# Kernel tuning notes

Measured on AMD Instinct MI355X. Metric: run time of the kernel, lower is better.

Reference implementation:

```python
import jax, jax.numpy as jnp
import numpy as np

N_HEAD = 16
EPS = 1e-6

def hypersphere_norm(x, g):
    # unit-normalize on hidden dim, rescale to sqrt(d), learnable gain
    d = x.shape[-1]
    n = jnp.linalg.norm(x, axis=-1, keepdims=True)
    return (x / (n + EPS)) * jnp.sqrt(jnp.asarray(d, x.dtype)) * g


def setup_inputs() -> dict:
    key = jax.random.key(0)
    ks = jax.random.split(key, 8)
    B, S, D, F = 2, 2048, 2048, 8192
    s = lambda fan: 1.0 / np.sqrt(fan)
    return {
        "hidden_states": jax.random.normal(ks[0], (B, S, D), jnp.float32),
        "Wq": jax.random.normal(ks[1], (D, D), jnp.float32) * s(D),
        "Wk": jax.random.normal(ks[2], (D, D), jnp.float32) * s(D),
        "Wv": jax.random.normal(ks[3], (D, D), jnp.float32) * s(D),
        "Wo": jax.random.normal(ks[4], (D, D), jnp.float32) * s(D),
        "W_in": jax.random.normal(ks[5], (F, D), jnp.float32) * s(D),
        "W_out": jax.random.normal(ks[6], (D, F), jnp.float32) * s(F),
        "qk_norm_factor": jnp.asarray(1.0 / np.sqrt(D // N_HEAD), jnp.float32),
        "g_attn": jnp.ones((D,), jnp.float32),
        "g_mlp": jnp.ones((D,), jnp.float32),
    }


def reference(hidden_states, Wq, Wk, Wv, Wo, W_in, W_out, qk_norm_factor, g_attn, g_mlp):
    B, S, D = hidden_states.shape
    H = N_HEAD
    hd = D // H

    # ---- pre-attn hypersphere norm ----
    residual = hidden_states
    x = hypersphere_norm(hidden_states, g_attn)

    def shape_heads(t):  # [B,S,D] -> [B,H,S,hd]
        return t.reshape(B, S, H, hd).transpose(0, 2, 1, 3)

    q = shape_heads(x @ Wq.T)
    k = shape_heads(x @ Wk.T)
    v = shape_heads(x @ Wv.T)

    # QK-norm: unit-normalize per head vector
    q = q / (jnp.linalg.norm(q, axis=-1, keepdims=True) + EPS)
    k = k / (jnp.linalg.norm(k, axis=-1, keepdims=True) + EPS)

    scores = jnp.einsum("bhqd,bhkd->bhqk", q, k) * qk_norm_factor
    causal = jnp.tril(jnp.ones((S, S), bool))
    scores = jnp.where(causal[None, None], scores, jnp.asarray(-jnp.inf, scores.dtype))
    probs = jax.nn.softmax(scores, axis=-1)
    attn = jnp.einsum("bhqk,bhkd->bhqd", probs, v)  # [B,H,S,hd]
    attn = attn.transpose(0, 2, 1, 3).reshape(B, S, D)
    attn = attn @ Wo.T  # dropout=0

    h = residual + attn

    # ---- MLP branch ----
    residual = h
    y = hypersphere_norm(h, g_mlp)
    y = jax.nn.gelu(y @ W_in.T, approximate=False)
    y = y @ W_out.T
    return residual + y
```

## Files before the change

### kernel.cpp

```cpp
#include <hip/hip_runtime.h>
#include <math.h>


typedef unsigned short ushort_t;
typedef __attribute__((ext_vector_type(8))) short short8;
typedef __attribute__((ext_vector_type(4))) short short4v;
typedef __attribute__((ext_vector_type(4))) float f32x4;

#define S_LEN 2048
#define D_DIM 2048
#define F_DIM 8192
#define NHEAD 16
#define HDIM 128
#define BATCH 2
#define MROWS (BATCH * S_LEN)

__device__ __forceinline__ float bf2f(ushort_t u) {
  union { unsigned int i; float f; } c; c.i = ((unsigned int)u) << 16; return c.f;
}
__device__ __forceinline__ ushort_t f2bf(float f) {
  union { unsigned int i; float f; } c; c.f = f;
  unsigned int u = c.i;
  unsigned int r = (u + 0x7FFFu + ((u >> 16) & 1u)) >> 16;
  return (ushort_t)r;
}
__device__ __forceinline__ void load_lds16(const ushort_t* g, ushort_t* l) {
  __builtin_amdgcn_global_load_lds((const __attribute__((address_space(1))) void*)g,
                                   (__attribute__((address_space(3))) void*)l,
                                   16, 0, 0);
}

__global__ __launch_bounds__(256) void f2b_all_kernel(const float* __restrict__ wq,
                                                      const float* __restrict__ wk,
                                                      const float* __restrict__ wv,
                                                      const float* __restrict__ wo,
                                                      const float* __restrict__ wi,
                                                      const float* __restrict__ wu,
                                                      ushort_t* __restrict__ out) {
  const size_t DD = (size_t)D_DIM * D_DIM;
  const size_t FD = (size_t)F_DIM * D_DIM;
  const size_t e = ((size_t)blockIdx.x * 256 + threadIdx.x) * 4;
  const float* src;
  size_t off;
  if (e < 4 * DD) {
    const int wsel = (int)(e >> 22);
    src = (wsel == 0) ? wq : (wsel == 1) ? wk : (wsel == 2) ? wv : wo;
    off = e & (DD - 1);
  } else if (e < 4 * DD + FD) {
    src = wi; off = e - 4 * DD;
  } else {
    src = wu; off = e - 4 * DD - FD;
  }
  float4 v = *(const float4*)(src + off);
  short4v o;
  o[0] = (short)f2bf(v.x); o[1] = (short)f2bf(v.y);
  o[2] = (short)f2bf(v.z); o[3] = (short)f2bf(v.w);
  *(short4v*)(out + e) = o;
}

__global__ __launch_bounds__(256) void hsnorm_kernel(const float* __restrict__ x,
                                                     const float* __restrict__ g,
                                                     ushort_t* __restrict__ out) {
  const int row = blockIdx.x;
  const int t = threadIdx.x;
  const size_t base = (size_t)row * D_DIM + t * 8;
  float4 x0 = *(const float4*)(x + base);
  float4 x1 = *(const float4*)(x + base + 4);
  float f[8] = {x0.x, x0.y, x0.z, x0.w, x1.x, x1.y, x1.z, x1.w};
  float ss = 0.f;
#pragma unroll
  for (int j = 0; j < 8; ++j) ss += f[j] * f[j];
#pragma unroll
  for (int o = 32; o >= 1; o >>= 1) ss += __shfl_xor(ss, o);
  __shared__ float red[4];
  if ((t & 63) == 0) red[t >> 6] = ss;
  __syncthreads();
  const float tot = red[0] + red[1] + red[2] + red[3];
  const float factor = 45.254833995939045f / (sqrtf(tot) + 1e-6f);
  float4 g0 = *(const float4*)(g + t * 8);
  float4 g1 = *(const float4*)(g + t * 8 + 4);
  float gg[8] = {g0.x, g0.y, g0.z, g0.w, g1.x, g1.y, g1.z, g1.w};
  short8 ov;
#pragma unroll
  for (int j = 0; j < 8; ++j) ov[j] = (short)f2bf(f[j] * factor * gg[j]);
  *(short8*)(out + base) = ov;
}

__global__ __launch_bounds__(256) void qknorm_kernel(ushort_t* __restrict__ buf, float scale) {
  const int wv = threadIdx.x >> 6;
  const int lane = threadIdx.x & 63;
  const size_t vi = (size_t)blockIdx.x * 4 + wv;
  ushort_t* p = buf + vi * 128 + lane * 2;
  const float a = bf2f(p[0]), b = bf2f(p[1]);
  float ss = a * a + b * b;
#pragma unroll
  for (int o = 32; o >= 1; o >>= 1) ss += __shfl_xor(ss, o);
  const float f = scale / (sqrtf(ss) + 1e-6f);
  p[0] = f2bf(a * f);
  p[1] = f2bf(b * f);
}

template <int EPI>
__global__ __launch_bounds__(256) void gemm_bt(const ushort_t* __restrict__ A,
                                               const ushort_t* __restrict__ W,
                                               const float* __restrict__ RES,
                                               void* __restrict__ Cv,
                                               int M, int N, int K) {
  __shared__ __align__(16) ushort_t a_lds[128 * 64];
  __shared__ __align__(16) ushort_t b_lds[128 * 64];
  const int tid = threadIdx.x;
  const int w = tid >> 6;
  const int lane = tid & 63;
  const int quad = lane >> 4;
  const int l15 = lane & 15;
  const int wr = w >> 1, wc = w & 1;
  const long bm = (long)blockIdx.x * 128;
  const long bn = (long)blockIdx.y * 128;

  const int srow = tid >> 2;
  const int scol = (tid & 3) * 8;
  const ushort_t* gA = A + (size_t)(bm + srow) * K + scol;
  const ushort_t* gB = W + (size_t)(bn + srow) * K + scol;
  ushort_t* lA = a_lds + w * 512;
  ushort_t* lB = b_lds + w * 512;
  const size_t half = (size_t)64 * K;

  f32x4 acc[4][4] = {};

  for (int k0 = 0; k0 < K; k0 += 64) {
    load_lds16(gA,             lA);
    load_lds16(gA + half,      lA + 2048);
    load_lds16(gB,             lB);
    load_lds16(gB + half,      lB + 2048);
    load_lds16(gA + 32,        lA + 4096);
    load_lds16(gA + 32 + half, lA + 6144);
    load_lds16(gB + 32,        lB + 4096);
    load_lds16(gB + 32 + half, lB + 6144);
    gA += 64; gB += 64;
    __syncthreads();
#pragma unroll
    for (int kk = 0; kk < 2; ++kk) {
      short8 af[4], bfr[4];
#pragma unroll
      for (int i = 0; i < 4; ++i) {
        af[i]  = *(const short8*)&a_lds[kk * 4096 + (wr * 64 + i * 16 + l15) * 32 + quad * 8];
        bfr[i] = *(const short8*)&b_lds[kk * 4096 + (wc * 64 + i * 16 + l15) * 32 + quad * 8];
      }
#pragma unroll
      for (int i = 0; i < 4; ++i)
#pragma unroll
        for (int j = 0; j < 4; ++j)
          acc[i][j] = __builtin_amdgcn_mfma_f32_16x16x32_bf16(af[i], bfr[j], acc[i][j], 0, 0, 0);
    }
    __syncthreads();
  }

  const size_t SZq = (size_t)MROWS * D_DIM;
#pragma unroll
  for (int i = 0; i < 4; ++i) {
    const long row0 = bm + wr * 64 + i * 16 + quad * 4;
#pragma unroll
    for (int j = 0; j < 4; ++j) {
      const long col = bn + wc * 64 + j * 16 + l15;
      if (EPI == 4) {
        if (col < 4096) {
          ushort_t* dst = (ushort_t*)Cv + (col < 2048 ? 0 : SZq);
          const long c = col & (D_DIM - 1);
#pragma unroll
          for (int r = 0; r < 4; ++r)
            dst[(size_t)(row0 + r) * D_DIM + c] = f2bf(acc[i][j][r]);
        } else {
          const long b = row0 >> 11;
          const long s0 = row0 & (S_LEN - 1);
          const long h = (col >> 7) & 15;
          const long d = col & (HDIM - 1);
          short4v ov;
#pragma unroll
          for (int r = 0; r < 4; ++r) ov[r] = (short)f2bf(acc[i][j][r]);
          *(short4v*)((ushort_t*)Cv + 2 * SZq + ((b * NHEAD + h) * HDIM + d) * S_LEN + s0) = ov;
        }
      } else {
#pragma unroll
        for (int r = 0; r < 4; ++r) {
          float v = acc[i][j][r];
          const size_t idx = (size_t)(row0 + r) * N + col;
          if (EPI == 1) {
            ((float*)Cv)[idx] = v + RES[idx];
          } else if (EPI == 2) {
            v = 0.5f * v * (1.0f + erff(v * 0.70710678118654752f));
            ((ushort_t*)Cv)[idx] = f2bf(v);
          }
        }
      }
    }
  }
}

__global__ __launch_bounds__(256) void attn_kernel(const ushort_t* __restrict__ q,
                                                   const ushort_t* __restrict__ k,
                                                   const ushort_t* __restrict__ vt,
                                                   ushort_t* __restrict__ out) {
  __shared__ __align__(16) ushort_t K_lds[64 * 128];
  __shared__ __align__(16) ushort_t Vt_lds[128 * 64];
  __shared__ __align__(16) ushort_t P_lds[4 * 16 * 64];
  const int tid = threadIdx.x;
  const int w = tid >> 6;
  const int lane = tid & 63;
  const int quad = lane >> 4;
  const int l15 = lane & 15;

  const int qt = (S_LEN / 64 - 1) - (blockIdx.x & (S_LEN / 64 - 1));
  const int bh = blockIdx.x >> 5;
  const int b = bh >> 4;
  const int h = bh & 15;
  const int q0 = qt * 64;
  const int wrow0 = q0 + w * 16;
  const size_t base = ((size_t)b * S_LEN) * D_DIM + h * HDIM;
  const size_t vtbase = ((size_t)(b * NHEAD + h)) * HDIM * S_LEN;

  short8 qa[4];
#pragma unroll
  for (int st = 0; st < 4; ++st)
    qa[st] = *(const short8*)(q + base + (size_t)(wrow0 + l15) * D_DIM + st * 32 + quad * 8);

  const int kc0 = w * 64 + lane;
  ushort_t* Pw = P_lds + w * 1024;

  f32x4 o[8] = {};
  float m[4], l[4];
#pragma unroll
  for (int r = 0; r < 4; ++r) { m[r] = -__builtin_inff(); l[r] = 0.f; }

  const int ktmax = (q0 + 63) >> 6;
  for (int kt = 0; kt <= ktmax; ++kt) {
#pragma unroll
    for (int r2 = 0; r2 < 4; ++r2) {
      const int c = r2 * 256 + kc0;
      {
        const int db = c >> 8, key = (c >> 2) & 63, dl = (c & 3) * 8;
        load_lds16(k + base + (size_t)(kt * 64 + key) * D_DIM + db * 32 + dl,
                   K_lds + (size_t)(r2 * 4 + w) * 512);
      }
      {
        const int kc = c >> 9, d = (c >> 2) & 127, kl = (c & 3) * 8;
        load_lds16(vt + vtbase + (size_t)d * S_LEN + kt * 64 + kc * 32 + kl,
                   Vt_lds + (size_t)(r2 * 4 + w) * 512);
      }
    }
    __syncthreads();

    if (kt * 64 <= wrow0 + 15) {
      f32x4 s[4];
#pragma unroll
      for (int h2 = 0; h2 < 4; ++h2) {
        f32x4 sa = {};
#pragma unroll
        for (int st = 0; st < 4; ++st) {
          short8 kb = *(const short8*)&K_lds[st * 2048 + (h2 * 16 + l15) * 32 + quad * 8];
          sa = __builtin_amdgcn_mfma_f32_16x16x32_bf16(qa[st], kb, sa, 0, 0, 0);
        }
        s[h2] = sa;
      }

      const int kbase = kt * 64 + l15;
      float alpha[4];
#pragma unroll
      for (int r = 0; r < 4; ++r) {
        const int qrow = wrow0 + quad * 4 + r;
        float sv[4];
#pragma unroll
        for (int h2 = 0; h2 < 4; ++h2)
          sv[h2] = (kbase + h2 * 16 <= qrow) ? s[h2][r] : -__builtin_inff();
        float tmax = fmaxf(fmaxf(sv[0], sv[1]), fmaxf(sv[2], sv[3]));
#pragma unroll
        for (int off = 8; off >= 1; off >>= 1) tmax = fmaxf(tmax, __shfl_xor(tmax, off));
        const float mn = fmaxf(m[r], tmax);
        const float al = __expf(m[r] - mn);
        float p[4], ps = 0.f;
#pragma unroll
        for (int h2 = 0; h2 < 4; ++h2) { p[h2] = __expf(sv[h2] - mn); ps += p[h2]; }
#pragma unroll
        for (int off = 8; off >= 1; off >>= 1) ps += __shfl_xor(ps, off);
        l[r] = l[r] * al + ps;
        m[r] = mn;
        alpha[r] = al;
#pragma unroll
        for (int h2 = 0; h2 < 4; ++h2)
          Pw[(h2 >> 1) * 512 + (quad * 4 + r) * 32 + (h2 & 1) * 16 + l15] = f2bf(p[h2]);
      }

#pragma unroll
      for (int c = 0; c < 8; ++c)
#pragma unroll
        for (int r = 0; r < 4; ++r) o[c][r] *= alpha[r];

      short8 af0 = *(const short8*)&Pw[l15 * 32 + quad * 8];
      short8 af1 = *(const short8*)&Pw[512 + l15 * 32 + quad * 8];
#pragma unroll
      for (int c = 0; c < 8; ++c) {
        short8 vb0 = *(const short8*)&Vt_lds[(c * 16 + l15) * 32 + quad * 8];
        o[c] = __builtin_amdgcn_mfma_f32_16x16x32_bf16(af0, vb0, o[c], 0, 0, 0);
        short8 vb1 = *(const short8*)&Vt_lds[4096 + (c * 16 + l15) * 32 + quad * 8];
        o[c] = __builtin_amdgcn_mfma_f32_16x16x32_bf16(af1, vb1, o[c], 0, 0, 0);
      }
    }
    __syncthreads();
  }

#pragma unroll
  for (int c = 0; c < 8; ++c)
#pragma unroll
    for (int r = 0; r < 4; ++r) {
      const float val = o[c][r] / l[r];
      out[base + (size_t)(wrow0 + quad * 4 + r) * D_DIM + c * 16 + l15] = f2bf(val);
    }
}

extern "C" void kernel_launch(void* const* d_in, const int* in_sizes, int n_in,
                              void* d_out, int out_size, void* d_ws, size_t ws_size,
                              hipStream_t stream) {
  const float* hid  = (const float*)d_in[0];
  const float* Wq   = (const float*)d_in[1];
  const float* Wk   = (const float*)d_in[2];
  const float* Wv   = (const float*)d_in[3];
  const float* Wo   = (const float*)d_in[4];
  const float* Win  = (const float*)d_in[5];
  const float* Wout = (const float*)d_in[6];
  const float* ga   = (const float*)d_in[8];
  const float* gm   = (const float*)d_in[9];
  float* out = (float*)d_out;

  const size_t DD = (size_t)D_DIM * D_DIM;
  const size_t FD = (size_t)F_DIM * D_DIM;
  const size_t SZ = (size_t)MROWS * D_DIM;

  ushort_t* wqb  = (ushort_t*)d_ws;
  ushort_t* wob  = wqb + 3 * DD;
  ushort_t* winb = wob + DD;
  ushort_t* woutb= winb + FD;
  float*    hb   = (float*)(woutb + FD);
  ushort_t* qb   = (ushort_t*)(hb + SZ);
  ushort_t* kb   = qb + SZ;
  ushort_t* vtb  = kb + SZ;
  ushort_t* xb   = vtb + SZ;
  ushort_t* mid  = kb;

  f2b_all_kernel<<<(unsigned)((4 * DD + 2 * FD) / 1024), 256, 0, stream>>>(
      Wq, Wk, Wv, Wo, Win, Wout, wqb);

  hsnorm_kernel<<<MROWS, 256, 0, stream>>>(hid, ga, xb);
  gemm_bt<4><<<dim3(MROWS / 128, 6144 / 128), 256, 0, stream>>>(
      xb, wqb, nullptr, qb, MROWS, 6144, D_DIM);
  qknorm_kernel<<<(MROWS * NHEAD) / 4, 256, 0, stream>>>(qb, 0.08838834764831845f);
  qknorm_kernel<<<(MROWS * NHEAD) / 4, 256, 0, stream>>>(kb, 1.0f);
  attn_kernel<<<BATCH * NHEAD * (S_LEN / 64), 256, 0, stream>>>(qb, kb, vtb, xb);
  gemm_bt<1><<<dim3(MROWS / 128, D_DIM / 128), 256, 0, stream>>>(
      xb, wob, hid, hb, MROWS, D_DIM, D_DIM);
  hsnorm_kernel<<<MROWS, 256, 0, stream>>>(hb, gm, qb);
  gemm_bt<2><<<dim3(MROWS / 128, F_DIM / 128), 256, 0, stream>>>(
      qb, winb, nullptr, mid, MROWS, F_DIM, D_DIM);
  gemm_bt<1><<<dim3(MROWS / 128, D_DIM / 128), 256, 0, stream>>>(
      mid, woutb, hb, out, MROWS, D_DIM, F_DIM);
}
```

Before: 994.7 us.

## Replace GEMM with 256x256-tile, double-buffered, swizzled-LDS 8-wave kernel

Replaces the 128x128 single-buffered GEMM with a 256x256 tile kernel using 512 threads, 128KB of dynamic LDS, and ping-pong buffers for the A and B stages. It adds XOR swizzling to avoid LDS bank conflicts, interleaves global-to-LDS loads with MFMA phases, and uses s_setprio around the compute sections. The goal is more data reuse per loaded byte and hiding memory latency behind compute. The trade-offs are higher register and LDS pressure and fewer blocks for the smaller GEMMs, e.g. 16x8 blocks for the D-by-D projections.

```diff
diff --git a/kernel.cpp b/kernel.cpp
--- a/kernel.cpp
+++ b/kernel.cpp
@@ -28,6 +28,9 @@
   __builtin_amdgcn_global_load_lds((const __attribute__((address_space(1))) void*)g,
                                    (__attribute__((address_space(3))) void*)l,
                                    16, 0, 0);
+}
+__device__ __forceinline__ f32x4 mf(short8 a, short8 b, f32x4 c) {
+  return __builtin_amdgcn_mfma_f32_16x16x32_bf16(a, b, c, 0, 0, 0);
 }
 
 __global__ __launch_bounds__(256) void f2b_all_kernel(const float* __restrict__ wq,
@@ -101,64 +104,148 @@
 }
 
 template <int EPI>
-__global__ __launch_bounds__(256) void gemm_bt(const ushort_t* __restrict__ A,
-                                               const ushort_t* __restrict__ W,
-                                               const float* __restrict__ RES,
-                                               void* __restrict__ Cv,
-                                               int M, int N, int K) {
-  __shared__ __align__(16) ushort_t a_lds[128 * 64];
-  __shared__ __align__(16) ushort_t b_lds[128 * 64];
+__global__ __launch_bounds__(512, 2) void gemm256(const ushort_t* __restrict__ A,
+                                                  const ushort_t* __restrict__ W,
+                                                  const float* __restrict__ RES,
+                                                  void* __restrict__ Cv,
+                                                  int M, int N, int K) {
+  extern __shared__ char smem[];
   const int tid = threadIdx.x;
   const int w = tid >> 6;
   const int lane = tid & 63;
   const int quad = lane >> 4;
   const int l15 = lane & 15;
-  const int wr = w >> 1, wc = w & 1;
-  const long bm = (long)blockIdx.x * 128;
-  const long bn = (long)blockIdx.y * 128;
-
-  const int srow = tid >> 2;
-  const int scol = (tid & 3) * 8;
-  const ushort_t* gA = A + (size_t)(bm + srow) * K + scol;
-  const ushort_t* gB = W + (size_t)(bn + srow) * K + scol;
-  ushort_t* lA = a_lds + w * 512;
-  ushort_t* lB = b_lds + w * 512;
-  const size_t half = (size_t)64 * K;
-
-  f32x4 acc[4][4] = {};
-
-  for (int k0 = 0; k0 < K; k0 += 64) {
-    load_lds16(gA,             lA);
-    load_lds16(gA + half,      lA + 2048);
-    load_lds16(gB,             lB);
-    load_lds16(gB + half,      lB + 2048);
-    load_lds16(gA + 32,        lA + 4096);
-    load_lds16(gA + 32 + half, lA + 6144);
-    load_lds16(gB + 32,        lB + 4096);
-    load_lds16(gB + 32 + half, lB + 6144);
-    gA += 64; gB += 64;
-    __syncthreads();
-#pragma unroll
-    for (int kk = 0; kk < 2; ++kk) {
-      short8 af[4], bfr[4];
+  const int wr = w >> 2, wc = w & 3;
+  const long bm = (long)blockIdx.x * 256;
+  const long bn = (long)blockIdx.y * 256;
+
+  const int sw = l15 & 7;
+  const int arow = (wr * 128 + l15) << 7;
+  const int a_off0 = arow + ((quad ^ sw) << 4);
+  const int a_off1 = arow + (((4 | quad) ^ sw) << 4);
+  const int brow = (wc * 64 + l15) << 7;
+  const int b_off0 = 65536 + brow + ((quad ^ sw) << 4);
+  const int b_off1 = 65536 + brow + (((4 | quad) ^ sw) << 4);
+
+  const int sr = tid >> 3;
+  const int ss = ((tid & 7) ^ (sr & 7)) << 3;
+  const ushort_t* gA = A + (size_t)(bm + sr) * K + ss;
+  const ushort_t* gB = W + (size_t)(bn + sr) * K + ss;
+  const size_t rstep = (size_t)64 * K;
+  const int sdst = w * 1024;
+
+#define STAGE_A(PB, GP)                                                        \
+  {                                                                            \
+    _Pragma("unroll") for (int ld = 0; ld < 4; ++ld)                           \
+        load_lds16((GP) + ld * rstep,                                          \
+                   (ushort_t*)(smem + (PB)*32768 + ld * 8192 + sdst));         \
+  }
+#define STAGE_B(PB, GP)                                                        \
+  {                                                                            \
+    _Pragma("unroll") for (int ld = 0; ld < 4; ++ld)                           \
+        load_lds16((GP) + ld * rstep,                                          \
+                   (ushort_t*)(smem + 65536 + (PB)*32768 + ld * 8192 + sdst)); \
+  }
+
+  f32x4 acc[8][4] = {};
+  short8 af[4][2], bf[4][2];
+  const int NT = K >> 6;
+
+  STAGE_A(0, gA);
+  STAGE_B(0, gB);
+  STAGE_A(1, gA + 64);
+  gA += 128;
+  gB += 64;
+  asm volatile("s_waitcnt vmcnt(4)" ::: "memory");
+  __builtin_amdgcn_s_barrier();
+
+  for (int kt0 = 0; kt0 < NT; kt0 += 2) {
+#pragma unroll
+    for (int pp = 0; pp < 2; ++pp) {
+      const int kt = kt0 + pp;
+      const char* sa = smem + pp * 32768;
 #pragma unroll
       for (int i = 0; i < 4; ++i) {
-        af[i]  = *(const short8*)&a_lds[kk * 4096 + (wr * 64 + i * 16 + l15) * 32 + quad * 8];
-        bfr[i] = *(const short8*)&b_lds[kk * 4096 + (wc * 64 + i * 16 + l15) * 32 + quad * 8];
-      }
+        af[i][0] = *(const short8*)(sa + a_off0 + i * 2048);
+        af[i][1] = *(const short8*)(sa + a_off1 + i * 2048);
+      }
+#pragma unroll
+      for (int j = 0; j < 2; ++j) {
+        bf[j][0] = *(const short8*)(sa + b_off0 + j * 2048);
+        bf[j][1] = *(const short8*)(sa + b_off1 + j * 2048);
+      }
+      if (kt + 1 < NT) STAGE_B(1 - pp, gB);
+      gB += 64;
+      __builtin_amdgcn_s_barrier();
+      __builtin_amdgcn_s_setprio(1);
 #pragma unroll
       for (int i = 0; i < 4; ++i)
 #pragma unroll
-        for (int j = 0; j < 4; ++j)
-          acc[i][j] = __builtin_amdgcn_mfma_f32_16x16x32_bf16(af[i], bfr[j], acc[i][j], 0, 0, 0);
+        for (int j = 0; j < 2; ++j) {
+          acc[i][j] = mf(af[i][0], bf[j][0], acc[i][j]);
+          acc[i][j] = mf(af[i][1], bf[j][1], acc[i][j]);
+        }
+      __builtin_amdgcn_s_setprio(0);
+      __builtin_amdgcn_s_barrier();
+#pragma unroll
+      for (int j = 0; j < 2; ++j) {
+        bf[2 + j][0] = *(const short8*)(sa + b_off0 + (2 + j) * 2048);
+        bf[2 + j][1] = *(const short8*)(sa + b_off1 + (2 + j) * 2048);
+      }
+      __builtin_amdgcn_s_barrier();
+      __builtin_amdgcn_s_setprio(1);
+#pragma unroll
+      for (int i = 0; i < 4; ++i)
+#pragma unroll
+        for (int j = 0; j < 2; ++j) {
+          acc[i][2 + j] = mf(af[i][0], bf[2 + j][0], acc[i][2 + j]);
+          acc[i][2 + j] = mf(af[i][1], bf[2 + j][1], acc[i][2 + j]);
+        }
+      __builtin_amdgcn_s_setprio(0);
+      __builtin_amdgcn_s_barrier();
+#pragma unroll
+      for (int i = 0; i < 4; ++i) {
+        af[i][0] = *(const short8*)(sa + a_off0 + (4 + i) * 2048);
+        af[i][1] = *(const short8*)(sa + a_off1 + (4 + i) * 2048);
+      }
+      __builtin_amdgcn_s_barrier();
+      __builtin_amdgcn_s_setprio(1);
+#pragma unroll
+      for (int i = 0; i < 4; ++i)
+#pragma unroll
+        for (int j = 0; j < 2; ++j) {
+          acc[4 + i][2 + j] = mf(af[i][0], bf[2 + j][0], acc[4 + i][2 + j]);
+          acc[4 + i][2 + j] = mf(af[i][1], bf[2 + j][1], acc[4 + i][2 + j]);
+        }
+      __builtin_amdgcn_s_setprio(0);
+      __builtin_amdgcn_s_barrier();
+      if (kt + 2 < NT) STAGE_A(pp, gA);
+      gA += 64;
+      __builtin_amdgcn_s_barrier();
+      __builtin_amdgcn_s_setprio(1);
+#pragma unroll
+      for (int i = 0; i < 4; ++i)
+#pragma unroll
+        for (int j = 0; j < 2; ++j) {
+          acc[4 + i][j] = mf(af[i][0], bf[j][0], acc[4 + i][j]);
+          acc[4 + i][j] = mf(af[i][1], bf[j][1], acc[4 + i][j]);
+        }
+      __builtin_amdgcn_s_setprio(0);
+      if (kt + 2 < NT) {
+        asm volatile("s_waitcnt vmcnt(4)" ::: "memory");
+      } else {
+        asm volatile("s_waitcnt vmcnt(0)" ::: "memory");
+      }
+      __builtin_amdgcn_s_barrier();
     }
-    __syncthreads();
-  }
+  }
+#undef STAGE_A
+#undef STAGE_B
 
   const size_t SZq = (size_t)MROWS * D_DIM;
 #pragma unroll
-  for (int i = 0; i < 4; ++i) {
-    const long row0 = bm + wr * 64 + i * 16 + quad * 4;
+  for (int i = 0; i < 8; ++i) {
+    const long row0 = bm + wr * 128 + i * 16 + quad * 4;
 #pragma unroll
     for (int j = 0; j < 4; ++j) {
       const long col = bn + wc * 64 + j * 16 + l15;
@@ -345,20 +432,31 @@
   ushort_t* xb   = vtb + SZ;
   ushort_t* mid  = kb;
 
+  static int attr_set = 0;
+  if (!attr_set) {
+    hipFuncSetAttribute((const void*)&gemm256<1>,
+                        hipFuncAttributeMaxDynamicSharedMemorySize, 131072);
+    hipFuncSetAttribute((const void*)&gemm256<2>,
+                        hipFuncAttributeMaxDynamicSharedMemorySize, 131072);
+    hipFuncSetAttribute((const void*)&gemm256<4>,
+                        hipFuncAttributeMaxDynamicSharedMemorySize, 131072);
+    attr_set = 1;
+  }
+
   f2b_all_kernel<<<(unsigned)((4 * DD + 2 * FD) / 1024), 256, 0, stream>>>(
       Wq, Wk, Wv, Wo, Win, Wout, wqb);
 
   hsnorm_kernel<<<MROWS, 256, 0, stream>>>(hid, ga, xb);
-  gemm_bt<4><<<dim3(MROWS / 128, 6144 / 128), 256, 0, stream>>>(
+  gemm256<4><<<dim3(MROWS / 256, 6144 / 256), 512, 131072, stream>>>(
       xb, wqb, nullptr, qb, MROWS, 6144, D_DIM);
   qknorm_kernel<<<(MROWS * NHEAD) / 4, 256, 0, stream>>>(qb, 0.08838834764831845f);
   qknorm_kernel<<<(MROWS * NHEAD) / 4, 256, 0, stream>>>(kb, 1.0f);
   attn_kernel<<<BATCH * NHEAD * (S_LEN / 64), 256, 0, stream>>>(qb, kb, vtb, xb);
-  gemm_bt<1><<<dim3(MROWS / 128, D_DIM / 128), 256, 0, stream>>>(
+  gemm256<1><<<dim3(MROWS / 256, D_DIM / 256), 512, 131072, stream>>>(
       xb, wob, hid, hb, MROWS, D_DIM, D_DIM);
   hsnorm_kernel<<<MROWS, 256, 0, stream>>>(hb, gm, qb);
-  gemm_bt<2><<<dim3(MROWS / 128, F_DIM / 128), 256, 0, stream>>>(
+  gemm256<2><<<dim3(MROWS / 256, F_DIM / 256), 512, 131072, stream>>>(
       qb, winb, nullptr, mid, MROWS, F_DIM, D_DIM);
-  gemm_bt<1><<<dim3(MROWS / 128, D_DIM / 128), 256, 0, stream>>>(
+  gemm256<1><<<dim3(MROWS / 256, D_DIM / 256), 512, 131072, stream>>>(
       mid, woutb, hb, out, MROWS, D_DIM, F_DIM);
 }
```

New measurement: 986.5 us. About the same (-0.8%).

## Replace GEMM with 256x256 tile, 4-stage LDS pipeline, swizzle and XCD block remap

Applied to the files above, without the earlier changes.

Replaces the 128x128 single-buffered GEMM with a 512-thread 256x256-tile kernel. It prefetches three K-steps ahead into a 4-deep LDS ring using explicit vmcnt waits and a single barrier per step. LDS layout is XOR-swizzled to reduce bank conflicts, and blocks are remapped so neighbouring tiles land on the same XCD for L2 reuse. The 128KB of dynamic LDS limits occupancy to one block per CU and increases register pressure from the 8x4 accumulators.

```diff
diff --git a/kernel.cpp b/kernel.cpp
--- a/kernel.cpp
+++ b/kernel.cpp
@@ -28,6 +28,9 @@
   __builtin_amdgcn_global_load_lds((const __attribute__((address_space(1))) void*)g,
                                    (__attribute__((address_space(3))) void*)l,
                                    16, 0, 0);
+}
+__device__ __forceinline__ f32x4 mf(short8 a, short8 b, f32x4 c) {
+  return __builtin_amdgcn_mfma_f32_16x16x32_bf16(a, b, c, 0, 0, 0);
 }
 
 __global__ __launch_bounds__(256) void f2b_all_kernel(const float* __restrict__ wq,
@@ -101,64 +104,95 @@
 }
 
 template <int EPI>
-__global__ __launch_bounds__(256) void gemm_bt(const ushort_t* __restrict__ A,
-                                               const ushort_t* __restrict__ W,
-                                               const float* __restrict__ RES,
-                                               void* __restrict__ Cv,
-                                               int M, int N, int K) {
-  __shared__ __align__(16) ushort_t a_lds[128 * 64];
-  __shared__ __align__(16) ushort_t b_lds[128 * 64];
+__global__ __launch_bounds__(512, 2) void gemm256(const ushort_t* __restrict__ A,
+                                                  const ushort_t* __restrict__ W,
+                                                  const float* __restrict__ RES,
+                                                  void* __restrict__ Cv,
+                                                  int M, int N, int K) {
+  extern __shared__ char smem[];
   const int tid = threadIdx.x;
   const int w = tid >> 6;
   const int lane = tid & 63;
   const int quad = lane >> 4;
   const int l15 = lane & 15;
-  const int wr = w >> 1, wc = w & 1;
-  const long bm = (long)blockIdx.x * 128;
-  const long bn = (long)blockIdx.y * 128;
-
+  const int wr = w >> 2, wc = w & 3;
+
+  const int bid = blockIdx.x;
+  const int cpx = gridDim.x >> 3;
+  const int wg = (bid & 7) * cpx + (bid >> 3);
+  const long bm = (long)(wg & 15) * 256;
+  const long bn = (long)(wg >> 4) * 256;
+
+  const int rx = (l15 >> 1) & 3;
+  const int a_base = ((wr * 128 + l15) << 6) + ((quad ^ rx) << 4);
+  const int b_base = ((wc * 64 + l15) << 6) + ((quad ^ rx) << 4);
+
+  const int sp = (((tid & 3) ^ ((tid >> 3) & 3)) << 3);
   const int srow = tid >> 2;
-  const int scol = (tid & 3) * 8;
-  const ushort_t* gA = A + (size_t)(bm + srow) * K + scol;
-  const ushort_t* gB = W + (size_t)(bn + srow) * K + scol;
-  ushort_t* lA = a_lds + w * 512;
-  ushort_t* lB = b_lds + w * 512;
-  const size_t half = (size_t)64 * K;
-
-  f32x4 acc[4][4] = {};
-
-  for (int k0 = 0; k0 < K; k0 += 64) {
-    load_lds16(gA,             lA);
-    load_lds16(gA + half,      lA + 2048);
-    load_lds16(gB,             lB);
-    load_lds16(gB + half,      lB + 2048);
-    load_lds16(gA + 32,        lA + 4096);
-    load_lds16(gA + 32 + half, lA + 6144);
-    load_lds16(gB + 32,        lB + 4096);
-    load_lds16(gB + 32 + half, lB + 6144);
-    gA += 64; gB += 64;
-    __syncthreads();
-#pragma unroll
-    for (int kk = 0; kk < 2; ++kk) {
-      short8 af[4], bfr[4];
-#pragma unroll
-      for (int i = 0; i < 4; ++i) {
-        af[i]  = *(const short8*)&a_lds[kk * 4096 + (wr * 64 + i * 16 + l15) * 32 + quad * 8];
-        bfr[i] = *(const short8*)&b_lds[kk * 4096 + (wc * 64 + i * 16 + l15) * 32 + quad * 8];
-      }
-#pragma unroll
-      for (int i = 0; i < 4; ++i)
-#pragma unroll
-        for (int j = 0; j < 4; ++j)
-          acc[i][j] = __builtin_amdgcn_mfma_f32_16x16x32_bf16(af[i], bfr[j], acc[i][j], 0, 0, 0);
+  const ushort_t* gA = A + (size_t)(bm + srow) * K + sp;
+  const ushort_t* gB = W + (size_t)(bn + srow) * K + sp;
+  const size_t rstep = (size_t)128 * K;
+  const int sdst = w * 1024;
+
+#define STAGE(BI, STEP)                                                     \
+  {                                                                         \
+    char* ab = smem + (BI)*16384;                                           \
+    char* bb = smem + 65536 + (BI)*16384;                                   \
+    const ushort_t* ga = gA + (size_t)(STEP) * 32;                          \
+    const ushort_t* gb = gB + (size_t)(STEP) * 32;                          \
+    load_lds16(ga, (ushort_t*)(ab + sdst));                                 \
+    load_lds16(ga + rstep, (ushort_t*)(ab + 8192 + sdst));                  \
+    load_lds16(gb, (ushort_t*)(bb + sdst));                                 \
+    load_lds16(gb + rstep, (ushort_t*)(bb + 8192 + sdst));                  \
+  }
+
+  f32x4 acc[8][4] = {};
+  short8 af[4], bf[4];
+  const int NT = K >> 5;
+
+  STAGE(0, 0);
+  STAGE(1, 1);
+  STAGE(2, 2);
+  asm volatile("s_waitcnt vmcnt(8)" ::: "memory");
+  __builtin_amdgcn_s_barrier();
+
+  for (int s = 0; s < NT; ++s) {
+    const char* sa = smem + (s & 3) * 16384;
+    const char* sb = smem + 65536 + (s & 3) * 16384;
+#pragma unroll
+    for (int j = 0; j < 4; ++j) bf[j] = *(const short8*)(sb + b_base + j * 1024);
+#pragma unroll
+    for (int i = 0; i < 4; ++i) af[i] = *(const short8*)(sa + a_base + i * 1024);
+    if (s + 3 < NT) STAGE((s + 3) & 3, s + 3);
+    __builtin_amdgcn_s_setprio(1);
+#pragma unroll
+    for (int i = 0; i < 4; ++i)
+#pragma unroll
+      for (int j = 0; j < 4; ++j) acc[i][j] = mf(af[i], bf[j], acc[i][j]);
+    __builtin_amdgcn_s_setprio(0);
+#pragma unroll
+    for (int i = 0; i < 4; ++i) af[i] = *(const short8*)(sa + a_base + (4 + i) * 1024);
+    __builtin_amdgcn_s_setprio(1);
+#pragma unroll
+    for (int i = 0; i < 4; ++i)
+#pragma unroll
+      for (int j = 0; j < 4; ++j) acc[4 + i][j] = mf(af[i], bf[j], acc[4 + i][j]);
+    __builtin_amdgcn_s_setprio(0);
+    if (s < NT - 3) {
+      asm volatile("s_waitcnt vmcnt(8)" ::: "memory");
+    } else if (s == NT - 3) {
+      asm volatile("s_waitcnt vmcnt(4)" ::: "memory");
+    } else {
+      asm volatile("s_waitcnt vmcnt(0)" ::: "memory");
     }
-    __syncthreads();
-  }
+    __builtin_amdgcn_s_barrier();
+  }
+#undef STAGE
 
   const size_t SZq = (size_t)MROWS * D_DIM;
 #pragma unroll
-  for (int i = 0; i < 4; ++i) {
-    const long row0 = bm + wr * 64 + i * 16 + quad * 4;
+  for (int i = 0; i < 8; ++i) {
+    const long row0 = bm + wr * 128 + i * 16 + quad * 4;
 #pragma unroll
     for (int j = 0; j < 4; ++j) {
       const long col = bn + wc * 64 + j * 16 + l15;
@@ -345,20 +379,31 @@
   ushort_t* xb   = vtb + SZ;
   ushort_t* mid  = kb;
 
+  static int attr_set = 0;
+  if (!attr_set) {
+    hipFuncSetAttribute((const void*)&gemm256<1>,
+                        hipFuncAttributeMaxDynamicSharedMemorySize, 131072);
+    hipFuncSetAttribute((const void*)&gemm256<2>,
+                        hipFuncAttributeMaxDynamicSharedMemorySize, 131072);
+    hipFuncSetAttribute((const void*)&gemm256<4>,
+                        hipFuncAttributeMaxDynamicSharedMemorySize, 131072);
+    attr_set = 1;
+  }
+
   f2b_all_kernel<<<(unsigned)((4 * DD + 2 * FD) / 1024), 256, 0, stream>>>(
       Wq, Wk, Wv, Wo, Win, Wout, wqb);
 
   hsnorm_kernel<<<MROWS, 256, 0, stream>>>(hid, ga, xb);
-  gemm_bt<4><<<dim3(MROWS / 128, 6144 / 128), 256, 0, stream>>>(
+  gemm256<4><<<(MROWS / 256) * (6144 / 256), 512, 131072, stream>>>(
       xb, wqb, nullptr, qb, MROWS, 6144, D_DIM);
   qknorm_kernel<<<(MROWS * NHEAD) / 4, 256, 0, stream>>>(qb, 0.08838834764831845f);
   qknorm_kernel<<<(MROWS * NHEAD) / 4, 256, 0, stream>>>(kb, 1.0f);
   attn_kernel<<<BATCH * NHEAD * (S_LEN / 64), 256, 0, stream>>>(qb, kb, vtb, xb);
-  gemm_bt<1><<<dim3(MROWS / 128, D_DIM / 128), 256, 0, stream>>>(
+  gemm256<1><<<(MROWS / 256) * (D_DIM / 256), 512, 131072, stream>>>(
       xb, wob, hid, hb, MROWS, D_DIM, D_DIM);
   hsnorm_kernel<<<MROWS, 256, 0, stream>>>(hb, gm, qb);
-  gemm_bt<2><<<dim3(MROWS / 128, F_DIM / 128), 256, 0, stream>>>(
+  gemm256<2><<<(MROWS / 256) * (F_DIM / 256), 512, 131072, stream>>>(
       qb, winb, nullptr, mid, MROWS, F_DIM, D_DIM);
-  gemm_bt<1><<<dim3(MROWS / 128, D_DIM / 128), 256, 0, stream>>>(
+  gemm256<1><<<(MROWS / 256) * (D_DIM / 256), 512, 131072, stream>>>(
       mid, woutb, hb, out, MROWS, D_DIM, F_DIM);
 }
```

New measurement: 1.011 ms. Within noise of the previous version (+1.6%).
